# Performance work log

Hardware: AMD Instinct MI355X
Metric: run time of the kernel (lower is better)

Reference implementation:

```python
import jax, jax.numpy as jnp
import numpy as np

TEMPERATURE = 0.1
TOP_K = 8


def setup_inputs() -> dict:
    key = jax.random.key(0)
    k1, k2, k3 = jax.random.split(key, 3)
    num_tokens, d_model, num_experts = 32768, 2048, 64
    x = jax.random.normal(k1, (num_tokens, d_model), dtype=jnp.float32)
    # nn.Linear default init: U(-1/sqrt(fan_in), 1/sqrt(fan_in))
    bound = 1.0 / np.sqrt(d_model)
    W = jax.random.uniform(k2, (num_experts, d_model), jnp.float32, -bound, bound)
    b = jax.random.uniform(k3, (num_experts,), jnp.float32, -bound, bound)
    return {"x": x, "W": W, "b": b}


def reference(x, W, b):
    # gate: [T, E] = x @ W^T + b, scaled by temperature
    routing_logits = (jnp.einsum('td,ed->te', x, W) + b) / TEMPERATURE
    routing_probs = jax.nn.softmax(routing_logits, axis=-1)
    top_k_probs, top_k_indices = jax.lax.top_k(routing_probs, TOP_K)
    top_k_probs_normalized = top_k_probs / jnp.sum(top_k_probs, axis=-1, keepdims=True)
    return routing_logits, top_k_probs_normalized, top_k_indices
```

## Files before the change

### kernel.cpp

```cpp
#include <hip/hip_runtime.h>
#include <cstdint>

#define T_TOKENS 32768
#define D_MODEL  2048
#define N_EXP    64
#define BM       64
#define BK       64
#define CHUNKS   (D_MODEL / BK)
#define LDK      (BK + 8)

typedef short bf16x8 __attribute__((ext_vector_type(8)));
typedef unsigned short u16x8 __attribute__((ext_vector_type(8)));
typedef float f32x4 __attribute__((ext_vector_type(4)));

__device__ __forceinline__ unsigned short f2bf(float f) {
    union { float f; unsigned int u; } c; c.f = f;
    unsigned int u = c.u;
    u += 0x7fffu + ((u >> 16) & 1u);
    return (unsigned short)(u >> 16);
}
__device__ __forceinline__ float bf2f(unsigned short h) {
    union { float f; unsigned int u; } c; c.u = ((unsigned int)h) << 16;
    return c.f;
}

__device__ __forceinline__ void split3(const float4& a, const float4& b,
                                       u16x8& h, u16x8& m, u16x8& l) {
    float f[8] = {a.x, a.y, a.z, a.w, b.x, b.y, b.z, b.w};
#pragma unroll
    for (int i = 0; i < 8; ++i) {
        unsigned short hh = f2bf(f[i]);
        float r1 = f[i] - bf2f(hh);
        unsigned short mm = f2bf(r1);
        float r2 = r1 - bf2f(mm);
        unsigned short ll = f2bf(r2);
        h[i] = hh; m[i] = mm; l[i] = ll;
    }
}

__global__ void router_prep(const float* __restrict__ W, unsigned short* __restrict__ Wpk) {
    const int t = blockIdx.x * 256 + threadIdx.x;
    const int lane = t & 63;
    const int sj = t >> 6;
    const int e  = (sj & 3) * 16 + (lane & 15);
    const int k0 = (sj >> 2) * 32 + (lane >> 4) * 8;
    const float* src = W + (size_t)e * D_MODEL + k0;
    float4 f0 = *(const float4*)src;
    float4 f1 = *(const float4*)(src + 4);
    u16x8 h, m, l;
    split3(f0, f1, h, m, l);
    unsigned short* dst = Wpk + (size_t)sj * 1536 + lane * 8;
    *(u16x8*)(dst)        = h;
    *(u16x8*)(dst + 512)  = m;
    *(u16x8*)(dst + 1024) = l;
}

#define LOADX(R, CH) do {                                                     \
    _Pragma("unroll") for (int p_ = 0; p_ < 2; ++p_) {                        \
        const float* s_ = xg + (size_t)p_ * 32 * D_MODEL + (CH) * BK;         \
        R[p_][0] = *(const float4*)s_;                                        \
        R[p_][1] = *(const float4*)(s_ + 4);                                  \
    } } while (0)

#define CONV(R, BUF) do {                                                     \
    _Pragma("unroll") for (int p_ = 0; p_ < 2; ++p_) {                        \
        u16x8 h_, m_, l_;                                                     \
        split3(R[p_][0], R[p_][1], h_, m_, l_);                               \
        const int o_ = (rid + p_ * 32) * LDK + kq * 8;                        \
        *(u16x8*)&Asm[BUF][0][o_] = h_;                                       \
        *(u16x8*)&Asm[BUF][1][o_] = m_;                                       \
        *(u16x8*)&Asm[BUF][2][o_] = l_;                                       \
    } } while (0)

#define COMPUTE(CH, BUF) do {                                                 \
    _Pragma("unroll") for (int ks_ = 0; ks_ < 2; ++ks_) {                     \
        const int ko_ = ks_ * 32 + kq8;                                       \
        bf16x8 ah_ = *(const bf16x8*)&Asm[BUF][0][aoff + ko_];                \
        bf16x8 am_ = *(const bf16x8*)&Asm[BUF][1][aoff + ko_];                \
        bf16x8 al_ = *(const bf16x8*)&Asm[BUF][2][aoff + ko_];                \
        _Pragma("unroll") for (int j_ = 0; j_ < 4; ++j_) {                    \
            const unsigned short* wq_ = wlane + (size_t)(((CH)*2 + ks_)*4 + j_) * 1536; \
            bf16x8 bh_ = *(const bf16x8*)(wq_);                               \
            bf16x8 bm_ = *(const bf16x8*)(wq_ + 512);                         \
            bf16x8 bl_ = *(const bf16x8*)(wq_ + 1024);                        \
            acc[j_] = __builtin_amdgcn_mfma_f32_16x16x32_bf16(ah_, bh_, acc[j_], 0, 0, 0); \
            acc[j_] = __builtin_amdgcn_mfma_f32_16x16x32_bf16(am_, bh_, acc[j_], 0, 0, 0); \
            acc[j_] = __builtin_amdgcn_mfma_f32_16x16x32_bf16(ah_, bm_, acc[j_], 0, 0, 0); \
            acc[j_] = __builtin_amdgcn_mfma_f32_16x16x32_bf16(al_, bh_, acc[j_], 0, 0, 0); \
            acc[j_] = __builtin_amdgcn_mfma_f32_16x16x32_bf16(am_, bm_, acc[j_], 0, 0, 0); \
            acc[j_] = __builtin_amdgcn_mfma_f32_16x16x32_bf16(ah_, bl_, acc[j_], 0, 0, 0); \
        }                                                                     \
    } } while (0)

__global__ __launch_bounds__(256, 2) void router_gemm(
    const float* __restrict__ x, const unsigned short* __restrict__ Wpk,
    const float* __restrict__ b, float* __restrict__ logits)
{
    __shared__ unsigned short Asm[2][3][BM * LDK];

    const int tid = threadIdx.x;
    const int t0  = blockIdx.x * BM;
    const int kq  = tid & 7;
    const int rid = tid >> 3;

    const float* xg = x + (size_t)(t0 + rid) * D_MODEL + kq * 8;

    const int lane = tid & 63;
    const int w    = tid >> 6;
    const int ln   = lane & 15;
    const int kq8  = (lane >> 4) * 8;
    const int aoff = (w * 16 + ln) * LDK;
    const unsigned short* wlane = Wpk + lane * 8;

    f32x4 acc[4];
#pragma unroll
    for (int j = 0; j < 4; ++j) acc[j] = (f32x4)(0.f);

    float4 ra[2][2], rb[2][2];

    LOADX(ra, 0);
    CONV(ra, 0);
    LOADX(rb, 1);
    __syncthreads();

    for (int cc = 0; cc < CHUNKS; cc += 2) {
        if (cc + 2 < CHUNKS) LOADX(ra, cc + 2);
        CONV(rb, 1);
        COMPUTE(cc, 0);
        __syncthreads();

        if (cc + 3 < CHUNKS) LOADX(rb, cc + 3);
        if (cc + 2 < CHUNKS) CONV(ra, 0);
        COMPUTE(cc + 1, 1);
        __syncthreads();
    }

    float bias[4];
#pragma unroll
    for (int j = 0; j < 4; ++j) bias[j] = b[j * 16 + ln];
    const int trow = w * 16 + (lane >> 4) * 4;
#pragma unroll
    for (int j = 0; j < 4; ++j) {
#pragma unroll
        for (int r = 0; r < 4; ++r) {
            float v = (acc[j][r] + bias[j]) / 0.1f;
            logits[(size_t)(t0 + trow + r) * N_EXP + j * 16 + ln] = v;
        }
    }
}

__global__ __launch_bounds__(256) void router_topk(
    const float* __restrict__ logits, float* __restrict__ probs, float* __restrict__ idxs)
{
    const int tid  = threadIdx.x;
    const int t    = blockIdx.x * 32 + (tid >> 3);
    const int s    = tid & 7;
    const int lane = tid & 63;

    const float* row = logits + (size_t)t * 64 + s * 8;
    float4 v0 = *(const float4*)row;
    float4 v1 = *(const float4*)(row + 4);
    float v[8] = {v0.x, v0.y, v0.z, v0.w, v1.x, v1.y, v1.z, v1.w};

    float sel_v = 0.f; int sel_i = 0;
#pragma unroll
    for (int p = 0; p < 8; ++p) {
        float bm = v[0]; int bi = s * 8;
#pragma unroll
        for (int i = 1; i < 8; ++i) {
            bool g = v[i] > bm;
            bm = g ? v[i] : bm;
            bi = g ? s * 8 + i : bi;
        }
#pragma unroll
        for (int d = 1; d < 8; d <<= 1) {
            float om = __shfl_xor(bm, d);
            int   oi = __shfl_xor(bi, d);
            bool take = (om > bm) || (om == bm && oi < bi);
            bm = take ? om : bm;
            bi = take ? oi : bi;
        }
        if (s == p) { sel_v = bm; sel_i = bi; }
#pragma unroll
        for (int i = 0; i < 8; ++i)
            if (s * 8 + i == bi) v[i] = -__builtin_inff();
    }

    float mx = __shfl(sel_v, lane & ~7);
    float wgt = expf(sel_v - mx);
    float sum = wgt;
#pragma unroll
    for (int d = 1; d < 8; d <<= 1) sum += __shfl_xor(sum, d);

    probs[(size_t)t * 8 + s] = wgt / sum;
    idxs [(size_t)t * 8 + s] = (float)sel_i;
}

extern "C" void kernel_launch(void* const* d_in, const int* in_sizes, int n_in,
                              void* d_out, int out_size, void* d_ws, size_t ws_size,
                              hipStream_t stream) {
    const float* x = (const float*)d_in[0];
    const float* W = (const float*)d_in[1];
    const float* b = (const float*)d_in[2];
    float* out    = (float*)d_out;
    float* logits = out;
    float* probs  = out + (size_t)T_TOKENS * N_EXP;
    float* idxs   = probs + (size_t)T_TOKENS * 8;
    unsigned short* Wpk = (unsigned short*)d_ws;

    router_prep<<<dim3(64),            dim3(256), 0, stream>>>(W, Wpk);
    router_gemm<<<dim3(T_TOKENS / BM), dim3(256), 0, stream>>>(x, Wpk, b, logits);
    router_topk<<<dim3(T_TOKENS / 32), dim3(256), 0, stream>>>(logits, probs, idxs);
}
```

Baseline: 428.0 us.

## Load x fragments directly into registers, drop LDS staging and barriers

The GEMM no longer stages x through shared memory. Each lane loads its own MFMA A-fragment straight from global memory, splits it into three bf16 parts in registers, and double-buffers both x and the W fragments in registers with no __syncthreads. Accumulation is split across several accumulators (two primary ones plus one for the correction terms) to break MFMA dependency chains. The intent is to remove LDS traffic and barrier stalls and to overlap loads with compute, at the cost of more registers and less coalesced, strided per-lane global reads of x.

```diff
diff --git a/kernel.cpp b/kernel.cpp
--- a/kernel.cpp
+++ b/kernel.cpp
@@ -4,13 +4,9 @@
 #define T_TOKENS 32768
 #define D_MODEL  2048
 #define N_EXP    64
-#define BM       64
-#define BK       64
-#define CHUNKS   (D_MODEL / BK)
-#define LDK      (BK + 8)
+#define KSTEPS   (D_MODEL / 32)
 
 typedef short bf16x8 __attribute__((ext_vector_type(8)));
-typedef unsigned short u16x8 __attribute__((ext_vector_type(8)));
 typedef float f32x4 __attribute__((ext_vector_type(4)));
 
 __device__ __forceinline__ unsigned short f2bf(float f) {
@@ -25,17 +21,18 @@
 }
 
 __device__ __forceinline__ void split3(const float4& a, const float4& b,
-                                       u16x8& h, u16x8& m, u16x8& l) {
+                                       bf16x8& h, bf16x8& m, bf16x8& l) {
     float f[8] = {a.x, a.y, a.z, a.w, b.x, b.y, b.z, b.w};
+    union { bf16x8 v; unsigned short s[8]; } H, M, L;
 #pragma unroll
     for (int i = 0; i < 8; ++i) {
         unsigned short hh = f2bf(f[i]);
         float r1 = f[i] - bf2f(hh);
         unsigned short mm = f2bf(r1);
         float r2 = r1 - bf2f(mm);
-        unsigned short ll = f2bf(r2);
-        h[i] = hh; m[i] = mm; l[i] = ll;
+        H.s[i] = hh; M.s[i] = mm; L.s[i] = f2bf(r2);
     }
+    h = H.v; m = M.v; l = L.v;
 }
 
 __global__ void router_prep(const float* __restrict__ W, unsigned short* __restrict__ Wpk) {
@@ -47,103 +44,80 @@
     const float* src = W + (size_t)e * D_MODEL + k0;
     float4 f0 = *(const float4*)src;
     float4 f1 = *(const float4*)(src + 4);
-    u16x8 h, m, l;
+    bf16x8 h, m, l;
     split3(f0, f1, h, m, l);
     unsigned short* dst = Wpk + (size_t)sj * 1536 + lane * 8;
-    *(u16x8*)(dst)        = h;
-    *(u16x8*)(dst + 512)  = m;
-    *(u16x8*)(dst + 1024) = l;
+    *(bf16x8*)(dst)        = h;
+    *(bf16x8*)(dst + 512)  = m;
+    *(bf16x8*)(dst + 1024) = l;
 }
 
-#define LOADX(R, CH) do {                                                     \
-    _Pragma("unroll") for (int p_ = 0; p_ < 2; ++p_) {                        \
-        const float* s_ = xg + (size_t)p_ * 32 * D_MODEL + (CH) * BK;         \
-        R[p_][0] = *(const float4*)s_;                                        \
-        R[p_][1] = *(const float4*)(s_ + 4);                                  \
+#define LOADS(A0, A1, BH, BM, BL, KS) do {                                    \
+    const float* ax_ = xg + (KS) * 32;                                        \
+    A0 = *(const float4*)ax_;                                                 \
+    A1 = *(const float4*)(ax_ + 4);                                           \
+    _Pragma("unroll") for (int j_ = 0; j_ < 4; ++j_) {                        \
+        const unsigned short* wq_ = wlane + (size_t)((KS) * 4 + j_) * 1536;   \
+        BH[j_] = *(const bf16x8*)wq_;                                         \
+        BM[j_] = *(const bf16x8*)(wq_ + 512);                                 \
+        BL[j_] = *(const bf16x8*)(wq_ + 1024);                                \
     } } while (0)
 
-#define CONV(R, BUF) do {                                                     \
-    _Pragma("unroll") for (int p_ = 0; p_ < 2; ++p_) {                        \
-        u16x8 h_, m_, l_;                                                     \
-        split3(R[p_][0], R[p_][1], h_, m_, l_);                               \
-        const int o_ = (rid + p_ * 32) * LDK + kq * 8;                        \
-        *(u16x8*)&Asm[BUF][0][o_] = h_;                                       \
-        *(u16x8*)&Asm[BUF][1][o_] = m_;                                       \
-        *(u16x8*)&Asm[BUF][2][o_] = l_;                                       \
-    } } while (0)
-
-#define COMPUTE(CH, BUF) do {                                                 \
-    _Pragma("unroll") for (int ks_ = 0; ks_ < 2; ++ks_) {                     \
-        const int ko_ = ks_ * 32 + kq8;                                       \
-        bf16x8 ah_ = *(const bf16x8*)&Asm[BUF][0][aoff + ko_];                \
-        bf16x8 am_ = *(const bf16x8*)&Asm[BUF][1][aoff + ko_];                \
-        bf16x8 al_ = *(const bf16x8*)&Asm[BUF][2][aoff + ko_];                \
-        _Pragma("unroll") for (int j_ = 0; j_ < 4; ++j_) {                    \
-            const unsigned short* wq_ = wlane + (size_t)(((CH)*2 + ks_)*4 + j_) * 1536; \
-            bf16x8 bh_ = *(const bf16x8*)(wq_);                               \
-            bf16x8 bm_ = *(const bf16x8*)(wq_ + 512);                         \
-            bf16x8 bl_ = *(const bf16x8*)(wq_ + 1024);                        \
-            acc[j_] = __builtin_amdgcn_mfma_f32_16x16x32_bf16(ah_, bh_, acc[j_], 0, 0, 0); \
-            acc[j_] = __builtin_amdgcn_mfma_f32_16x16x32_bf16(am_, bh_, acc[j_], 0, 0, 0); \
-            acc[j_] = __builtin_amdgcn_mfma_f32_16x16x32_bf16(ah_, bm_, acc[j_], 0, 0, 0); \
-            acc[j_] = __builtin_amdgcn_mfma_f32_16x16x32_bf16(al_, bh_, acc[j_], 0, 0, 0); \
-            acc[j_] = __builtin_amdgcn_mfma_f32_16x16x32_bf16(am_, bm_, acc[j_], 0, 0, 0); \
-            acc[j_] = __builtin_amdgcn_mfma_f32_16x16x32_bf16(ah_, bl_, acc[j_], 0, 0, 0); \
-        }                                                                     \
+#define COMP(A0, A1, BH, BM, BL, ACCP) do {                                   \
+    bf16x8 ah_, am_, al_;                                                     \
+    split3(A0, A1, ah_, am_, al_);                                            \
+    _Pragma("unroll") for (int j_ = 0; j_ < 4; ++j_) {                        \
+        ACCP[j_] = __builtin_amdgcn_mfma_f32_16x16x32_bf16(ah_, BH[j_], ACCP[j_], 0, 0, 0); \
+        accC[j_] = __builtin_amdgcn_mfma_f32_16x16x32_bf16(am_, BH[j_], accC[j_], 0, 0, 0); \
+        accC[j_] = __builtin_amdgcn_mfma_f32_16x16x32_bf16(ah_, BM[j_], accC[j_], 0, 0, 0); \
+        accC[j_] = __builtin_amdgcn_mfma_f32_16x16x32_bf16(al_, BH[j_], accC[j_], 0, 0, 0); \
+        accC[j_] = __builtin_amdgcn_mfma_f32_16x16x32_bf16(am_, BM[j_], accC[j_], 0, 0, 0); \
+        accC[j_] = __builtin_amdgcn_mfma_f32_16x16x32_bf16(ah_, BL[j_], accC[j_], 0, 0, 0); \
     } } while (0)
 
 __global__ __launch_bounds__(256, 2) void router_gemm(
     const float* __restrict__ x, const unsigned short* __restrict__ Wpk,
     const float* __restrict__ b, float* __restrict__ logits)
 {
-    __shared__ unsigned short Asm[2][3][BM * LDK];
-
-    const int tid = threadIdx.x;
-    const int t0  = blockIdx.x * BM;
-    const int kq  = tid & 7;
-    const int rid = tid >> 3;
-
-    const float* xg = x + (size_t)(t0 + rid) * D_MODEL + kq * 8;
-
+    const int tid  = threadIdx.x;
     const int lane = tid & 63;
     const int w    = tid >> 6;
+    const int t0   = blockIdx.x * 64 + w * 16;
     const int ln   = lane & 15;
-    const int kq8  = (lane >> 4) * 8;
-    const int aoff = (w * 16 + ln) * LDK;
+
+    const float* xg = x + (size_t)(t0 + ln) * D_MODEL + (lane >> 4) * 8;
     const unsigned short* wlane = Wpk + lane * 8;
 
-    f32x4 acc[4];
+    f32x4 accP0[4], accP1[4], accC[4];
 #pragma unroll
-    for (int j = 0; j < 4; ++j) acc[j] = (f32x4)(0.f);
+    for (int j = 0; j < 4; ++j) {
+        accP0[j] = (f32x4)(0.f); accP1[j] = (f32x4)(0.f); accC[j] = (f32x4)(0.f);
+    }
 
-    float4 ra[2][2], rb[2][2];
+    float4 a00, a01, a10, a11;
+    bf16x8 bh0[4], bm0[4], bl0[4], bh1[4], bm1[4], bl1[4];
 
-    LOADX(ra, 0);
-    CONV(ra, 0);
-    LOADX(rb, 1);
-    __syncthreads();
+    LOADS(a00, a01, bh0, bm0, bl0, 0);
+    LOADS(a10, a11, bh1, bm1, bl1, 1);
 
-    for (int cc = 0; cc < CHUNKS; cc += 2) {
-        if (cc + 2 < CHUNKS) LOADX(ra, cc + 2);
-        CONV(rb, 1);
-        COMPUTE(cc, 0);
-        __syncthreads();
-
-        if (cc + 3 < CHUNKS) LOADX(rb, cc + 3);
-        if (cc + 2 < CHUNKS) CONV(ra, 0);
-        COMPUTE(cc + 1, 1);
-        __syncthreads();
+    for (int ks = 0; ks < KSTEPS - 2; ks += 2) {
+        COMP(a00, a01, bh0, bm0, bl0, accP0);
+        LOADS(a00, a01, bh0, bm0, bl0, ks + 2);
+        COMP(a10, a11, bh1, bm1, bl1, accP1);
+        LOADS(a10, a11, bh1, bm1, bl1, ks + 3);
     }
+    COMP(a00, a01, bh0, bm0, bl0, accP0);
+    COMP(a10, a11, bh1, bm1, bl1, accP1);
 
     float bias[4];
 #pragma unroll
     for (int j = 0; j < 4; ++j) bias[j] = b[j * 16 + ln];
-    const int trow = w * 16 + (lane >> 4) * 4;
+    const int trow = (lane >> 4) * 4;
 #pragma unroll
     for (int j = 0; j < 4; ++j) {
 #pragma unroll
         for (int r = 0; r < 4; ++r) {
-            float v = (acc[j][r] + bias[j]) / 0.1f;
+            float v = (accP0[j][r] + accP1[j][r] + (accC[j][r] + bias[j])) / 0.1f;
             logits[(size_t)(t0 + trow + r) * N_EXP + j * 16 + ln] = v;
         }
     }
@@ -208,7 +182,7 @@
     float* idxs   = probs + (size_t)T_TOKENS * 8;
     unsigned short* Wpk = (unsigned short*)d_ws;
 
-    router_prep<<<dim3(64),            dim3(256), 0, stream>>>(W, Wpk);
-    router_gemm<<<dim3(T_TOKENS / BM), dim3(256), 0, stream>>>(x, Wpk, b, logits);
-    router_topk<<<dim3(T_TOKENS / 32), dim3(256), 0, stream>>>(logits, probs, idxs);
+    router_prep<<<dim3(64),             dim3(256), 0, stream>>>(W, Wpk);
+    router_gemm<<<dim3(T_TOKENS / 64),  dim3(256), 0, stream>>>(x, Wpk, b, logits);
+    router_topk<<<dim3(T_TOKENS / 32),  dim3(256), 0, stream>>>(logits, probs, idxs);
 }
```

Measured after the change: 419.4 us. -2.0%, faster.
